# Performance work log

Measured on AMD Instinct MI355X. Metric: run time of the kernel, lower is better.

The kernel has to match this reference:

```python
import jax, jax.numpy as jnp
import numpy as np

IN_FEATURES = 4096
PADDED_DIM = 4096
K_HALF = PADDED_DIM // 2 + 1  # 2049
K = K_HALF
ALPHA_INIT = 1.0
INIT_SCALE = 0.1
BIAS_SCALE = 0.1
BATCH = 8192


def setup_inputs() -> dict:
    key = jax.random.key(0)
    kx, kr, ki, kb = jax.random.split(key, 4)
    x = jax.random.normal(kx, (BATCH, IN_FEATURES), dtype=jnp.float32)
    # Params initialized as in the module's __init__ (frequency-decayed scale)
    k_idx = jnp.arange(K_HALF, dtype=jnp.float32)
    prior_s = 1.0 / jnp.sqrt(1.0 + k_idx ** ALPHA_INIT)
    w_real = jax.random.normal(kr, (K_HALF,), dtype=jnp.float32) * (INIT_SCALE * prior_s)
    w_imag = jax.random.normal(ki, (K_HALF,), dtype=jnp.float32) * (INIT_SCALE * prior_s)
    w_imag = w_imag.at[0].set(0.0)
    w_imag = w_imag.at[-1].set(0.0)  # Nyquist bin (padded_dim even)
    bias = jax.random.normal(kb, (PADDED_DIM,), dtype=jnp.float32) * BIAS_SCALE
    return {"x": x, "w_real": w_real, "w_imag": w_imag, "bias": bias}


def _fourier_full(w_real, w_imag):
    # Mask frequencies >= K, then build full-length spectrum via Hermitian symmetry.
    mask = (jnp.arange(K_HALF) < K).astype(w_real.dtype)
    half = w_real * mask + 1j * (w_imag * mask)  # [k_half] complex
    nyq = half[-1].real[None].astype(half.dtype)  # real Nyquist bin
    full = jnp.concatenate([half[:-1], nyq, jnp.conj(half[1:-1])[::-1]])  # [padded_dim]
    return full


def reference(x, w_real, w_imag, bias):
    fft_full = _fourier_full(w_real, w_imag)  # [padded_dim] complex64
    # d_in == padded_dim -> no zero-padding needed (slice is a no-op, kept faithful)
    x_pad = x[..., :PADDED_DIM]
    Xf = jnp.fft.fft(x_pad, axis=-1)                 # [B, padded_dim] complex
    y = jnp.fft.ifft(Xf * fft_full[None, :], axis=-1).real  # [B, padded_dim]
    return y + bias[None, :]
```

## Files before the change

### kernel.cpp

```cpp
#include <hip/hip_runtime.h>
#include <math.h>

#define N 4096
#define THREADS 256
#define BATCH 8192

#define SWZ(i) ((i) ^ (((i) >> 4) & 15))
#define IDX16(p) ((((p) & 3) << 2) | ((p) >> 2))

__device__ __forceinline__ float2 cmul(float2 a, float2 b) {
    return make_float2(fmaf(a.x, b.x, -(a.y * b.y)), fmaf(a.x, b.y, a.y * b.x));
}

template<bool INV>
__device__ __forceinline__ void dft4(float2* v, int base, int stride) {
    float2 a = v[base], b = v[base + stride], c = v[base + 2 * stride], d = v[base + 3 * stride];
    float2 t0 = make_float2(a.x + c.x, a.y + c.y);
    float2 t1 = make_float2(a.x - c.x, a.y - c.y);
    float2 t2 = make_float2(b.x + d.x, b.y + d.y);
    float2 t3 = make_float2(b.x - d.x, b.y - d.y);
    float2 j3 = INV ? make_float2(-t3.y, t3.x) : make_float2(t3.y, -t3.x);
    v[base]              = make_float2(t0.x + t2.x, t0.y + t2.y);
    v[base + stride]     = make_float2(t1.x + j3.x, t1.y + j3.y);
    v[base + 2 * stride] = make_float2(t0.x - t2.x, t0.y - t2.y);
    v[base + 3 * stride] = make_float2(t1.x - j3.x, t1.y - j3.y);
}

template<bool INV>
__device__ __forceinline__ void tw16(float2* v) {
    const float C1 = 0.9238795325112867f;
    const float S1 = 0.3826834323650898f;
    const float R2 = 0.7071067811865476f;
    const float s = INV ? 1.0f : -1.0f;
    const float2 W1 = make_float2(C1, s * S1);
    const float2 W2 = make_float2(R2, s * R2);
    const float2 W3 = make_float2(S1, s * C1);
    const float2 W6 = make_float2(-R2, s * R2);
    const float2 W9 = make_float2(-C1, -s * S1);
    v[5]  = cmul(v[5],  W1);
    v[9]  = cmul(v[9],  W2);
    v[13] = cmul(v[13], W3);
    v[6]  = cmul(v[6],  W2);
    { float2 z = v[10]; v[10] = INV ? make_float2(-z.y, z.x) : make_float2(z.y, -z.x); }
    v[14] = cmul(v[14], W6);
    v[7]  = cmul(v[7],  W3);
    v[11] = cmul(v[11], W6);
    v[15] = cmul(v[15], W9);
}

template<bool INV>
__device__ __forceinline__ void dft16(float2* v) {
    #pragma unroll
    for (int n1 = 0; n1 < 4; ++n1) dft4<INV>(v, n1, 4);
    tw16<INV>(v);
    #pragma unroll
    for (int k2 = 0; k2 < 4; ++k2) dft4<INV>(v, 4 * k2, 1);
}

template<bool INV>
__device__ __forceinline__ void dft16_perm(float2* v) {
    #pragma unroll
    for (int n1 = 0; n1 < 4; ++n1) dft4<INV>(v, 4 * n1, 1);
    tw16<INV>(v);
    #pragma unroll
    for (int k2 = 0; k2 < 4; ++k2) dft4<INV>(v, k2, 4);
}

__global__ void prep_kernel(const float* __restrict__ wr, const float* __restrict__ wi,
                            float2* __restrict__ H, float2* __restrict__ tw) {
    int i = blockIdx.x * blockDim.x + threadIdx.x;
    if (i < N) {
        double ang = -2.0 * M_PI * (double)i / (double)N;
        tw[i] = make_float2((float)cos(ang), (float)sin(ang));
        float re, im;
        if (i <= N / 2) {
            re = wr[i];
            im = (i == N / 2) ? 0.0f : wi[i];
        } else {
            re = wr[N - i];
            im = -wi[N - i];
        }
        H[i] = make_float2(re, im);
    }
}

__global__ void prep_twA_kernel(float2* __restrict__ twA) {
    int i = blockIdx.x * blockDim.x + threadIdx.x;
    int p = i >> 8, t = i & 255;
    double ang = -2.0 * M_PI * (double)(t * p) / (double)N;
    twA[i] = make_float2((float)cos(ang), (float)sin(ang));
}

__global__ __launch_bounds__(THREADS, 4) void fft_conv_kernel(
        const float* __restrict__ x, const float2* __restrict__ H,
        const float2* __restrict__ tw, const float2* __restrict__ twA,
        const float* __restrict__ bias, float* __restrict__ out) {
    __shared__ float2 lds[N];
    const int t = threadIdx.x;
    const long base1 = (long)(2 * blockIdx.x) * N;
    const long base2 = base1 + N;

    float2 v[16];

    #pragma unroll
    for (int r = 0; r < 16; ++r) {
        v[r].x = x[base1 + t + 256 * r];
        v[r].y = x[base2 + t + 256 * r];
    }

    dft16<false>(v);
    #pragma unroll
    for (int p = 1; p < 16; ++p)
        v[IDX16(p)] = cmul(v[IDX16(p)], twA[p * 256 + t]);
    #pragma unroll
    for (int p = 0; p < 16; ++p)
        lds[SWZ(16 * t + p)] = v[IDX16(p)];
    __syncthreads();

    #pragma unroll
    for (int r = 0; r < 16; ++r) v[r] = lds[SWZ(t + 256 * r)];
    __syncthreads();
    dft16<false>(v);
    {
        const int k = t & 15, j = t >> 4;
        #pragma unroll
        for (int p = 1; p < 16; ++p)
            v[IDX16(p)] = cmul(v[IDX16(p)], tw[16 * j * p]);
        #pragma unroll
        for (int p = 0; p < 16; ++p)
            lds[SWZ(k + 256 * j + 16 * p)] = v[IDX16(p)];
    }
    __syncthreads();

    #pragma unroll
    for (int r = 0; r < 16; ++r) v[r] = lds[SWZ(t + 256 * r)];
    __syncthreads();
    dft16<false>(v);
    #pragma unroll
    for (int q = 0; q < 16; ++q)
        v[q] = cmul(v[q], H[t + 256 * IDX16(q)]);

    dft16_perm<true>(v);
    #pragma unroll
    for (int p = 1; p < 16; ++p) {
        float2 w = twA[p * 256 + t]; w.y = -w.y;
        v[p] = cmul(v[p], w);
    }
    #pragma unroll
    for (int p = 0; p < 16; ++p)
        lds[SWZ(16 * t + p)] = v[p];
    __syncthreads();

    #pragma unroll
    for (int r = 0; r < 16; ++r) v[r] = lds[SWZ(t + 256 * r)];
    __syncthreads();
    dft16<true>(v);
    {
        const int k = t & 15, j = t >> 4;
        #pragma unroll
        for (int p = 1; p < 16; ++p) {
            float2 w = tw[16 * j * p]; w.y = -w.y;
            v[IDX16(p)] = cmul(v[IDX16(p)], w);
        }
        #pragma unroll
        for (int p = 0; p < 16; ++p)
            lds[SWZ(k + 256 * j + 16 * p)] = v[IDX16(p)];
    }
    __syncthreads();

    #pragma unroll
    for (int r = 0; r < 16; ++r) v[r] = lds[SWZ(t + 256 * r)];
    dft16<true>(v);
    const float inv = 1.0f / (float)N;
    #pragma unroll
    for (int p = 0; p < 16; ++p) {
        float2 val = v[IDX16(p)];
        float bb = bias[t + 256 * p];
        out[base1 + t + 256 * p] = fmaf(val.x, inv, bb);
        out[base2 + t + 256 * p] = fmaf(val.y, inv, bb);
    }
}

extern "C" void kernel_launch(void* const* d_in, const int* in_sizes, int n_in,
                              void* d_out, int out_size, void* d_ws, size_t ws_size,
                              hipStream_t stream) {
    const float* x  = (const float*)d_in[0];
    const float* wr = (const float*)d_in[1];
    const float* wi = (const float*)d_in[2];
    const float* bs = (const float*)d_in[3];
    float* out = (float*)d_out;

    float2* H   = (float2*)d_ws;
    float2* tw  = (float2*)((char*)d_ws + (size_t)N * sizeof(float2));
    float2* twA = (float2*)((char*)d_ws + (size_t)2 * N * sizeof(float2));

    prep_kernel<<<dim3(N / THREADS), dim3(THREADS), 0, stream>>>(wr, wi, H, tw);
    prep_twA_kernel<<<dim3(N / THREADS), dim3(THREADS), 0, stream>>>(twA);
    fft_conv_kernel<<<dim3(BATCH / 2), dim3(THREADS), 0, stream>>>(x, H, tw, twA, bs, out);
}
```

Before: 310.7 us.

## Process two complex FFT pairs per block to amortize twiddle and filter loads

Each block now handles four real rows, packed as two complex signals in separate LDS buffers, instead of two. Twiddle and filter loads are shared across both signals, and the grid is halved. This trims redundant global loads of tw/twA/H and the per-block overhead. In exchange it doubles register use (32 float2 live) and LDS to 64 KB per block, with launch bounds lowered to 2 blocks per SM, so occupancy and latency hiding may drop.

```diff
diff --git a/kernel.cpp b/kernel.cpp
--- a/kernel.cpp
+++ b/kernel.cpp
@@ -91,93 +91,134 @@
     twA[i] = make_float2((float)cos(ang), (float)sin(ang));
 }
 
-__global__ __launch_bounds__(THREADS, 4) void fft_conv_kernel(
+__global__ __launch_bounds__(THREADS, 2) void fft_conv_kernel(
         const float* __restrict__ x, const float2* __restrict__ H,
         const float2* __restrict__ tw, const float2* __restrict__ twA,
         const float* __restrict__ bias, float* __restrict__ out) {
-    __shared__ float2 lds[N];
+    __shared__ float2 lds[2 * N];
+    float2* __restrict__ ldsA = lds;
+    float2* __restrict__ ldsB = lds + N;
     const int t = threadIdx.x;
-    const long base1 = (long)(2 * blockIdx.x) * N;
+    const long base1 = (long)(4 * blockIdx.x) * N;
     const long base2 = base1 + N;
-
-    float2 v[16];
+    const long base3 = base1 + 2 * N;
+    const long base4 = base1 + 3 * N;
+
+    float2 va[16], vb[16];
 
     #pragma unroll
     for (int r = 0; r < 16; ++r) {
-        v[r].x = x[base1 + t + 256 * r];
-        v[r].y = x[base2 + t + 256 * r];
-    }
-
-    dft16<false>(v);
-    #pragma unroll
-    for (int p = 1; p < 16; ++p)
-        v[IDX16(p)] = cmul(v[IDX16(p)], twA[p * 256 + t]);
-    #pragma unroll
-    for (int p = 0; p < 16; ++p)
-        lds[SWZ(16 * t + p)] = v[IDX16(p)];
-    __syncthreads();
-
-    #pragma unroll
-    for (int r = 0; r < 16; ++r) v[r] = lds[SWZ(t + 256 * r)];
-    __syncthreads();
-    dft16<false>(v);
+        va[r].x = x[base1 + t + 256 * r];
+        va[r].y = x[base2 + t + 256 * r];
+    }
+    #pragma unroll
+    for (int r = 0; r < 16; ++r) {
+        vb[r].x = x[base3 + t + 256 * r];
+        vb[r].y = x[base4 + t + 256 * r];
+    }
+
+    dft16<false>(va);
+    dft16<false>(vb);
+    #pragma unroll
+    for (int p = 1; p < 16; ++p) {
+        float2 w = twA[p * 256 + t];
+        va[IDX16(p)] = cmul(va[IDX16(p)], w);
+        vb[IDX16(p)] = cmul(vb[IDX16(p)], w);
+    }
+    #pragma unroll
+    for (int p = 0; p < 16; ++p) ldsA[SWZ(16 * t + p)] = va[IDX16(p)];
+    #pragma unroll
+    for (int p = 0; p < 16; ++p) ldsB[SWZ(16 * t + p)] = vb[IDX16(p)];
+    __syncthreads();
+
+    #pragma unroll
+    for (int r = 0; r < 16; ++r) va[r] = ldsA[SWZ(t + 256 * r)];
+    #pragma unroll
+    for (int r = 0; r < 16; ++r) vb[r] = ldsB[SWZ(t + 256 * r)];
+    __syncthreads();
+    dft16<false>(va);
+    dft16<false>(vb);
     {
         const int k = t & 15, j = t >> 4;
         #pragma unroll
-        for (int p = 1; p < 16; ++p)
-            v[IDX16(p)] = cmul(v[IDX16(p)], tw[16 * j * p]);
-        #pragma unroll
-        for (int p = 0; p < 16; ++p)
-            lds[SWZ(k + 256 * j + 16 * p)] = v[IDX16(p)];
-    }
-    __syncthreads();
-
-    #pragma unroll
-    for (int r = 0; r < 16; ++r) v[r] = lds[SWZ(t + 256 * r)];
-    __syncthreads();
-    dft16<false>(v);
-    #pragma unroll
-    for (int q = 0; q < 16; ++q)
-        v[q] = cmul(v[q], H[t + 256 * IDX16(q)]);
-
-    dft16_perm<true>(v);
+        for (int p = 1; p < 16; ++p) {
+            float2 w = tw[16 * j * p];
+            va[IDX16(p)] = cmul(va[IDX16(p)], w);
+            vb[IDX16(p)] = cmul(vb[IDX16(p)], w);
+        }
+        #pragma unroll
+        for (int p = 0; p < 16; ++p) ldsA[SWZ(k + 256 * j + 16 * p)] = va[IDX16(p)];
+        #pragma unroll
+        for (int p = 0; p < 16; ++p) ldsB[SWZ(k + 256 * j + 16 * p)] = vb[IDX16(p)];
+    }
+    __syncthreads();
+
+    #pragma unroll
+    for (int r = 0; r < 16; ++r) va[r] = ldsA[SWZ(t + 256 * r)];
+    #pragma unroll
+    for (int r = 0; r < 16; ++r) vb[r] = ldsB[SWZ(t + 256 * r)];
+    __syncthreads();
+    dft16<false>(va);
+    dft16<false>(vb);
+    #pragma unroll
+    for (int q = 0; q < 16; ++q) {
+        float2 h = H[t + 256 * IDX16(q)];
+        va[q] = cmul(va[q], h);
+        vb[q] = cmul(vb[q], h);
+    }
+
+    dft16_perm<true>(va);
+    dft16_perm<true>(vb);
     #pragma unroll
     for (int p = 1; p < 16; ++p) {
         float2 w = twA[p * 256 + t]; w.y = -w.y;
-        v[p] = cmul(v[p], w);
-    }
-    #pragma unroll
-    for (int p = 0; p < 16; ++p)
-        lds[SWZ(16 * t + p)] = v[p];
-    __syncthreads();
-
-    #pragma unroll
-    for (int r = 0; r < 16; ++r) v[r] = lds[SWZ(t + 256 * r)];
-    __syncthreads();
-    dft16<true>(v);
+        va[p] = cmul(va[p], w);
+        vb[p] = cmul(vb[p], w);
+    }
+    #pragma unroll
+    for (int p = 0; p < 16; ++p) ldsA[SWZ(16 * t + p)] = va[p];
+    #pragma unroll
+    for (int p = 0; p < 16; ++p) ldsB[SWZ(16 * t + p)] = vb[p];
+    __syncthreads();
+
+    #pragma unroll
+    for (int r = 0; r < 16; ++r) va[r] = ldsA[SWZ(t + 256 * r)];
+    #pragma unroll
+    for (int r = 0; r < 16; ++r) vb[r] = ldsB[SWZ(t + 256 * r)];
+    __syncthreads();
+    dft16<true>(va);
+    dft16<true>(vb);
     {
         const int k = t & 15, j = t >> 4;
         #pragma unroll
         for (int p = 1; p < 16; ++p) {
             float2 w = tw[16 * j * p]; w.y = -w.y;
-            v[IDX16(p)] = cmul(v[IDX16(p)], w);
+            va[IDX16(p)] = cmul(va[IDX16(p)], w);
+            vb[IDX16(p)] = cmul(vb[IDX16(p)], w);
         }
         #pragma unroll
-        for (int p = 0; p < 16; ++p)
-            lds[SWZ(k + 256 * j + 16 * p)] = v[IDX16(p)];
-    }
-    __syncthreads();
-
-    #pragma unroll
-    for (int r = 0; r < 16; ++r) v[r] = lds[SWZ(t + 256 * r)];
-    dft16<true>(v);
+        for (int p = 0; p < 16; ++p) ldsA[SWZ(k + 256 * j + 16 * p)] = va[IDX16(p)];
+        #pragma unroll
+        for (int p = 0; p < 16; ++p) ldsB[SWZ(k + 256 * j + 16 * p)] = vb[IDX16(p)];
+    }
+    __syncthreads();
+
+    #pragma unroll
+    for (int r = 0; r < 16; ++r) va[r] = ldsA[SWZ(t + 256 * r)];
+    #pragma unroll
+    for (int r = 0; r < 16; ++r) vb[r] = ldsB[SWZ(t + 256 * r)];
+    dft16<true>(va);
+    dft16<true>(vb);
     const float inv = 1.0f / (float)N;
     #pragma unroll
     for (int p = 0; p < 16; ++p) {
-        float2 val = v[IDX16(p)];
+        float2 a = va[IDX16(p)];
+        float2 b = vb[IDX16(p)];
         float bb = bias[t + 256 * p];
-        out[base1 + t + 256 * p] = fmaf(val.x, inv, bb);
-        out[base2 + t + 256 * p] = fmaf(val.y, inv, bb);
+        out[base1 + t + 256 * p] = fmaf(a.x, inv, bb);
+        out[base2 + t + 256 * p] = fmaf(a.y, inv, bb);
+        out[base3 + t + 256 * p] = fmaf(b.x, inv, bb);
+        out[base4 + t + 256 * p] = fmaf(b.y, inv, bb);
     }
 }
 
@@ -196,5 +237,5 @@
 
     prep_kernel<<<dim3(N / THREADS), dim3(THREADS), 0, stream>>>(wr, wi, H, tw);
     prep_twA_kernel<<<dim3(N / THREADS), dim3(THREADS), 0, stream>>>(twA);
-    fft_conv_kernel<<<dim3(BATCH / 2), dim3(THREADS), 0, stream>>>(x, H, tw, twA, bs, out);
-}
+    fft_conv_kernel<<<dim3(BATCH / 4), dim3(THREADS), 0, stream>>>(x, H, tw, twA, bs, out);
+}
```

Measured after the change: 263.7 us. 1.18x faster.
